# Kernel optimization log

Hardware: AMD Instinct MI355X
Metric: run time of the kernel (lower is better)

The kernel has to match this reference:

```python
import jax, jax.numpy as jnp
import numpy as np

N_NODES = 100000
N_EDGES = 1600000
F_IN_N = 64
F_IN_E = 64
F_OUT_N = 64
F_OUT_E = 64


def setup_inputs() -> dict:
    key = jax.random.key(0)
    ks = jax.random.split(key, 10)
    nfeats = jax.random.normal(ks[0], (N_NODES, F_IN_N), dtype=jnp.float32)
    efeats = jax.random.normal(ks[1], (N_EDGES, F_IN_E), dtype=jnp.float32)
    src = jax.random.randint(ks[2], (N_EDGES,), 0, N_NODES, dtype=jnp.int32)
    dst = jax.random.randint(ks[3], (N_EDGES,), 0, N_NODES, dtype=jnp.int32)
    s = 0.05
    W_node = jax.random.normal(ks[4], (F_OUT_N, F_IN_N), dtype=jnp.float32) * s
    b_node = jnp.zeros((F_OUT_N,), dtype=jnp.float32)
    W_ni = jax.random.normal(ks[5], (F_OUT_E, F_IN_N), dtype=jnp.float32) * s
    W_nj = jax.random.normal(ks[6], (F_OUT_E, F_IN_N), dtype=jnp.float32) * s
    W_fij = jax.random.normal(ks[7], (F_OUT_E, F_IN_E), dtype=jnp.float32) * s
    bias = jnp.zeros((F_OUT_E,), dtype=jnp.float32)
    return {"nfeats": nfeats, "efeats": efeats, "src": src, "dst": dst,
            "W_node": W_node, "b_node": b_node, "W_ni": W_ni, "W_nj": W_nj,
            "W_fij": W_fij, "bias": bias}


def reference(nfeats, efeats, src, dst, W_node, b_node, W_ni, W_nj, W_fij, bias):
    # edge update: leaky_relu(f_ni[src] + f_nj[dst] + f_fij + bias)
    f_ni = nfeats @ W_ni.T        # [N, Fe]
    f_nj = nfeats @ W_nj.T        # [N, Fe]
    f_fij = efeats @ W_fij.T      # [E, Fe]
    f_out = jax.nn.leaky_relu(f_ni[src] + f_nj[dst] + f_fij + bias, negative_slope=0.01)
    # node update: mean over in-edges of transformed source features
    h = nfeats @ W_node.T + b_node                      # [N, Fn]
    msg_sum = jax.ops.segment_sum(h[src], dst, num_segments=N_NODES)   # [N, Fn]
    deg = jax.ops.segment_sum(jnp.ones((src.shape[0],), dtype=h.dtype), dst,
                              num_segments=N_NODES)
    h_out = msg_sum / jnp.maximum(deg, 1.0)[:, None]    # 0 for isolated nodes
    return (h_out, f_out)
```

## Files before the change

kernel.cpp:

```cpp
#include <hip/hip_runtime.h>

#define NN 100000
#define NE 1600000
#define F 64
#define NSB ((NN + 255) / 256)
#define NTB ((NN + 127) / 128)

typedef float f32x4 __attribute__((ext_vector_type(4)));
typedef short bf16x8 __attribute__((ext_vector_type(8)));

__device__ inline unsigned short f2bf(float f) {
    unsigned u = __builtin_bit_cast(unsigned, f);
    u = (u + 0x7fffu + ((u >> 16) & 1u)) >> 16;
    return (unsigned short)u;
}
__device__ inline float bf2f(unsigned short b) { return __builtin_bit_cast(float, (unsigned)b << 16); }
__device__ inline float bflo(unsigned u) { return __builtin_bit_cast(float, u << 16); }
__device__ inline float bfhi(unsigned u) { return __builtin_bit_cast(float, u & 0xffff0000u); }

__device__ inline bf16x8 pack8(const f32x4 v0, const f32x4 v1) {
    bf16x8 pk;
    pk[0] = (short)f2bf(v0[0]); pk[1] = (short)f2bf(v0[1]);
    pk[2] = (short)f2bf(v0[2]); pk[3] = (short)f2bf(v0[3]);
    pk[4] = (short)f2bf(v1[0]); pk[5] = (short)f2bf(v1[1]);
    pk[6] = (short)f2bf(v1[2]); pk[7] = (short)f2bf(v1[3]);
    return pk;
}

__global__ __launch_bounds__(256, 2) void node_kernel(
    const float* __restrict__ nfeats,
    const float* __restrict__ W_node, const float* __restrict__ b_node,
    const float* __restrict__ W_ni,   const float* __restrict__ W_nj,
    unsigned short* __restrict__ f_ni16, unsigned short* __restrict__ f_nj16,
    unsigned short* __restrict__ h16, int* __restrict__ counts)
{
    __shared__ bf16x8 As8[128 * 8];
    __shared__ bf16x8 Ws8[64 * 8];
    float* Df = reinterpret_cast<float*>(As8);

    const int t = threadIdx.x;
    const int w = t >> 6, lane = t & 63;
    const int tile0 = blockIdx.x * 128;
    const int m = blockIdx.y;

    if (m == 0 && t < 128 && tile0 + t < NN) counts[tile0 + t] = 0;

    {
        const float* Wp = (m == 0) ? W_ni : (m == 1) ? W_nj : W_node;
        const f32x4* gw = reinterpret_cast<const f32x4*>(Wp);
#pragma unroll
        for (int i = 0; i < 2; ++i) {
            const int c = i * 256 + t;
            const int row = c >> 3, slot = c & 7;
            Ws8[row * 8 + (slot ^ (row & 7))] = pack8(gw[2 * c], gw[2 * c + 1]);
        }
    }
    {
        const f32x4* gsrc = reinterpret_cast<const f32x4*>(nfeats + (size_t)tile0 * F);
#pragma unroll
        for (int i = 0; i < 4; ++i) {
            const int c = i * 256 + t;
            const int row = c >> 3, slot = c & 7;
            f32x4 v0 = f32x4{0.f, 0.f, 0.f, 0.f}, v1 = f32x4{0.f, 0.f, 0.f, 0.f};
            if (tile0 + row < NN) { v0 = gsrc[2 * c]; v1 = gsrc[2 * c + 1]; }
            As8[row * 8 + (slot ^ (row & 7))] = pack8(v0, v1);
        }
    }
    __syncthreads();

    bf16x8 af[2][2];
#pragma unroll
    for (int mt = 0; mt < 2; ++mt)
#pragma unroll
        for (int ks = 0; ks < 2; ++ks) {
            const int row = w * 32 + mt * 16 + (lane & 15);
            const int kslot = ks * 4 + (lane >> 4);
            af[mt][ks] = As8[row * 8 + (kslot ^ (row & 7))];
        }

    bf16x8 bfr[4][2];
#pragma unroll
    for (int nt = 0; nt < 4; ++nt)
#pragma unroll
        for (int ks = 0; ks < 2; ++ks) {
            const int c = nt * 16 + (lane & 15);
            const int kslot = ks * 4 + (lane >> 4);
            bfr[nt][ks] = Ws8[c * 8 + (kslot ^ (c & 7))];
        }

    f32x4 acc[2][4];
#pragma unroll
    for (int mt = 0; mt < 2; ++mt)
#pragma unroll
        for (int nt = 0; nt < 4; ++nt) acc[mt][nt] = f32x4{0.f, 0.f, 0.f, 0.f};
#pragma unroll
    for (int ks = 0; ks < 2; ++ks)
#pragma unroll
        for (int mt = 0; mt < 2; ++mt)
#pragma unroll
            for (int nt = 0; nt < 4; ++nt)
                acc[mt][nt] = __builtin_amdgcn_mfma_f32_16x16x32_bf16(
                    af[mt][ks], bfr[nt][ks], acc[mt][nt], 0, 0, 0);

    __syncthreads();

    unsigned short* outp = (m == 0) ? f_ni16 : (m == 1) ? f_nj16 : h16;

#pragma unroll
    for (int half = 0; half < 2; ++half) {
#pragma unroll
        for (int mt = 0; mt < 2; ++mt)
#pragma unroll
            for (int ntl = 0; ntl < 2; ++ntl) {
#pragma unroll
                for (int r = 0; r < 4; ++r) {
                    const int row = w * 32 + mt * 16 + (lane >> 4) * 4 + r;
                    const int col = ntl * 16 + (lane & 15);
                    float v = acc[mt][half * 2 + ntl][r];
                    if (m == 2) v += b_node[half * 32 + col];
                    Df[row * 32 + ((col + row) & 31)] = v;
                }
            }
        __syncthreads();

#pragma unroll
        for (int i = 0; i < 2; ++i) {
            const int idx = i * 256 + t;
            const int row = idx >> 2;
            const int c8 = (idx & 3) << 3;
            if (tile0 + row < NN) {
                const float* b = Df + row * 32;
                uint4 pk;
                unsigned u[4];
#pragma unroll
                for (int p = 0; p < 4; ++p) {
                    const unsigned lo = f2bf(b[(c8 + 2 * p + 0 + row) & 31]);
                    const unsigned hi = f2bf(b[(c8 + 2 * p + 1 + row) & 31]);
                    u[p] = lo | (hi << 16);
                }
                pk.x = u[0]; pk.y = u[1]; pk.z = u[2]; pk.w = u[3];
                *reinterpret_cast<uint4*>(outp + (size_t)(tile0 + row) * F + half * 32 + c8) = pk;
            }
        }
        __syncthreads();
    }
}

__global__ __launch_bounds__(256) void edge_kernel(
    const float* __restrict__ efeats,
    const int* __restrict__ src, const int* __restrict__ dst,
    const unsigned short* __restrict__ f_ni16, const unsigned short* __restrict__ f_nj16,
    const float* __restrict__ W_fij, const float* __restrict__ bias,
    float* __restrict__ f_out, int* __restrict__ counts)
{
    __shared__ bf16x8 As8[256 * 8];
    __shared__ bf16x8 Ws8[64 * 8];
    float* Df = reinterpret_cast<float*>(As8);

    const int t = threadIdx.x;
    const int w = t >> 6, lane = t & 63;
    const int tile0 = blockIdx.x * 256;
    const int e = tile0 + t;
    const int s = src[e], d = dst[e];

    atomicAdd(&counts[d], 1);

    {
        const f32x4* gw = reinterpret_cast<const f32x4*>(W_fij);
#pragma unroll
        for (int i = 0; i < 2; ++i) {
            const int c = i * 256 + t;
            const int row = c >> 3, slot = c & 7;
            Ws8[row * 8 + (slot ^ (row & 7))] = pack8(gw[2 * c], gw[2 * c + 1]);
        }
    }
    {
        const f32x4* gsrc = reinterpret_cast<const f32x4*>(efeats + (size_t)tile0 * F);
#pragma unroll
        for (int i = 0; i < 8; ++i) {
            const int c = i * 256 + t;
            const int row = c >> 3, slot = c & 7;
            const f32x4 v0 = __builtin_nontemporal_load(gsrc + 2 * c);
            const f32x4 v1 = __builtin_nontemporal_load(gsrc + 2 * c + 1);
            As8[row * 8 + (slot ^ (row & 7))] = pack8(v0, v1);
        }
    }
    const uint4* gi = reinterpret_cast<const uint4*>(f_ni16 + (size_t)s * F);
    const uint4* gj = reinterpret_cast<const uint4*>(f_nj16 + (size_t)d * F);
    uint4 vni[4], vnj[4];
#pragma unroll
    for (int i = 0; i < 4; ++i) { vni[i] = gi[i]; vnj[i] = gj[i]; }

    __syncthreads();

    bf16x8 af[4][2], bfr[4][2];
#pragma unroll
    for (int mt = 0; mt < 4; ++mt)
#pragma unroll
        for (int ks = 0; ks < 2; ++ks) {
            const int row = w * 64 + mt * 16 + (lane & 15);
            const int kslot = ks * 4 + (lane >> 4);
            af[mt][ks] = As8[row * 8 + (kslot ^ (row & 7))];
        }
#pragma unroll
    for (int nt = 0; nt < 4; ++nt)
#pragma unroll
        for (int ks = 0; ks < 2; ++ks) {
            const int c = nt * 16 + (lane & 15);
            const int kslot = ks * 4 + (lane >> 4);
            bfr[nt][ks] = Ws8[c * 8 + (kslot ^ (c & 7))];
        }

    f32x4 acc[4][4];
#pragma unroll
    for (int mt = 0; mt < 4; ++mt)
#pragma unroll
        for (int nt = 0; nt < 4; ++nt) acc[mt][nt] = f32x4{0.f, 0.f, 0.f, 0.f};

#pragma unroll
    for (int ks = 0; ks < 2; ++ks)
#pragma unroll
        for (int mt = 0; mt < 4; ++mt)
#pragma unroll
            for (int nt = 0; nt < 4; ++nt)
                acc[mt][nt] = __builtin_amdgcn_mfma_f32_16x16x32_bf16(
                    af[mt][ks], bfr[nt][ks], acc[mt][nt], 0, 0, 0);

    __syncthreads();

    f32x4* gout = reinterpret_cast<f32x4*>(f_out + (size_t)tile0 * F);

#pragma unroll
    for (int half = 0; half < 2; ++half) {
#pragma unroll
        for (int mt = 0; mt < 4; ++mt)
#pragma unroll
            for (int ntl = 0; ntl < 2; ++ntl) {
                const int nt = half * 2 + ntl;
#pragma unroll
                for (int r = 0; r < 4; ++r) {
                    const int row = w * 64 + mt * 16 + (lane >> 4) * 4 + r;
                    const int col = ntl * 16 + (lane & 15);
                    Df[row * 32 + ((col + row) & 31)] = acc[mt][nt][r];
                }
            }
        uint4 nni[4], nnj[4];
        if (half == 0) {
#pragma unroll
            for (int i = 0; i < 4; ++i) { nni[i] = gi[4 + i]; nnj[i] = gj[4 + i]; }
        }
        __syncthreads();

        float* rb = Df + t * 32;
#pragma unroll
        for (int c = 0; c < 32; ++c) {
            float v = rb[(c + t) & 31];
            const unsigned wi = vni[c >> 3][(c >> 1) & 3];
            const unsigned wj = vnj[c >> 3][(c >> 1) & 3];
            v += (c & 1) ? bfhi(wi) : bflo(wi);
            v += (c & 1) ? bfhi(wj) : bflo(wj);
            v += bias[half * 32 + c];
            v = (v > 0.f) ? v : 0.01f * v;
            rb[(c + t) & 31] = v;
        }
        __syncthreads();

#pragma unroll
        for (int i = 0; i < 8; ++i) {
            const int idx = i * 256 + t;
            const int row = idx >> 3;
            const int c4 = (idx & 7) << 2;
            const float* b = Df + row * 32;
            f32x4 v;
            v[0] = b[(c4 + 0 + row) & 31];
            v[1] = b[(c4 + 1 + row) & 31];
            v[2] = b[(c4 + 2 + row) & 31];
            v[3] = b[(c4 + 3 + row) & 31];
            __builtin_nontemporal_store(v, gout + row * 16 + half * 8 + (idx & 7));
        }
        if (half == 0) {
            __syncthreads();
#pragma unroll
            for (int i = 0; i < 4; ++i) { vni[i] = nni[i]; vnj[i] = nnj[i]; }
        }
    }
}

__global__ __launch_bounds__(256) void scan1_kernel(
    const int* __restrict__ counts, int* __restrict__ offsets, int* __restrict__ blocksums)
{
    __shared__ int sd[256];
    const int t = threadIdx.x;
    const int i = blockIdx.x * 256 + t;
    const int v = (i < NN) ? counts[i] : 0;
    sd[t] = v;
    __syncthreads();
#pragma unroll
    for (int off = 1; off < 256; off <<= 1) {
        const int x = (t >= off) ? sd[t - off] : 0;
        __syncthreads();
        sd[t] += x;
        __syncthreads();
    }
    if (i < NN) offsets[i] = sd[t] - v;
    if (t == 255) blocksums[blockIdx.x] = sd[255];
}

__global__ __launch_bounds__(512) void scan2_kernel(
    const int* __restrict__ blocksums, int* __restrict__ blockpref)
{
    __shared__ int sd[512];
    const int t = threadIdx.x;
    const int v = (t < NSB) ? blocksums[t] : 0;
    sd[t] = v;
    __syncthreads();
#pragma unroll
    for (int off = 1; off < 512; off <<= 1) {
        const int x = (t >= off) ? sd[t - off] : 0;
        __syncthreads();
        sd[t] += x;
        __syncthreads();
    }
    if (t < NSB) blockpref[t] = sd[t] - v;
}

__global__ __launch_bounds__(256) void scan3_kernel(
    int* __restrict__ offsets, const int* __restrict__ blockpref, int* __restrict__ cursor)
{
    const int i = blockIdx.x * 256 + threadIdx.x;
    if (i < NN) {
        const int o = offsets[i] + blockpref[blockIdx.x];
        offsets[i] = o;
        cursor[i] = o;
    }
    if (i == 0) offsets[NN] = NE;
}

__global__ __launch_bounds__(256) void place_kernel(
    const int* __restrict__ src, const int* __restrict__ dst,
    int* __restrict__ cursor, int* __restrict__ eidx)
{
    const int e = blockIdx.x * 256 + threadIdx.x;
    if (e >= NE) return;
    const int pos = atomicAdd(&cursor[dst[e]], 1);
    eidx[pos] = src[e];
}

__global__ __launch_bounds__(256) void gather_kernel(
    const unsigned short* __restrict__ h16, const int* __restrict__ offsets,
    const int* __restrict__ eidx, float* __restrict__ h_out)
{
    const int n = blockIdx.x * 4 + (threadIdx.x >> 6);
    const int lane = threadIdx.x & 63;
    if (n >= NN) return;
    const int beg = offsets[n], end = offsets[n + 1];
    float acc = 0.f;
    int k = beg;
    for (; k + 4 <= end; k += 4) {
        const int s0 = eidx[k], s1 = eidx[k + 1], s2 = eidx[k + 2], s3 = eidx[k + 3];
        const float v0 = bf2f(h16[(size_t)s0 * F + lane]);
        const float v1 = bf2f(h16[(size_t)s1 * F + lane]);
        const float v2 = bf2f(h16[(size_t)s2 * F + lane]);
        const float v3 = bf2f(h16[(size_t)s3 * F + lane]);
        acc += v0; acc += v1; acc += v2; acc += v3;
    }
    for (; k < end; ++k) acc += bf2f(h16[(size_t)eidx[k] * F + lane]);
    const float deg = (float)(end - beg);
    __builtin_nontemporal_store(acc / fmaxf(deg, 1.0f), h_out + (size_t)n * F + lane);
}

extern "C" void kernel_launch(void* const* d_in, const int* in_sizes, int n_in,
                              void* d_out, int out_size, void* d_ws, size_t ws_size,
                              hipStream_t stream)
{
    const float* nfeats = (const float*)d_in[0];
    const float* efeats = (const float*)d_in[1];
    const int*   src    = (const int*)  d_in[2];
    const int*   dst    = (const int*)  d_in[3];
    const float* W_node = (const float*)d_in[4];
    const float* b_node = (const float*)d_in[5];
    const float* W_ni   = (const float*)d_in[6];
    const float* W_nj   = (const float*)d_in[7];
    const float* W_fij  = (const float*)d_in[8];
    const float* bias   = (const float*)d_in[9];

    float* h_out = (float*)d_out;
    float* f_out = (float*)d_out + (size_t)NN * F;

    unsigned short* f_ni16 = (unsigned short*)d_ws;
    unsigned short* f_nj16 = f_ni16 + (size_t)NN * F;
    unsigned short* h16    = f_nj16 + (size_t)NN * F;
    int*   offsets = (int*)(h16 + (size_t)NN * F);
    int*   cursor  = offsets + (NN + 1);
    int*   counts  = cursor + NN;
    int*   eidx    = counts + NN;
    int*   blocksums = eidx + NE;
    int*   blockpref = blocksums + NSB;
    const size_t need = ((size_t)3 * NN * F) * sizeof(unsigned short)
                      + ((size_t)(3 * NN + 1) + NE + 2 * NSB) * sizeof(int);
    if (ws_size < need) return;

    node_kernel<<<dim3(NTB, 3), 256, 0, stream>>>(nfeats, W_node, b_node, W_ni, W_nj,
                                                  f_ni16, f_nj16, h16, counts);
    edge_kernel<<<NE / 256, 256, 0, stream>>>(efeats, src, dst, f_ni16, f_nj16, W_fij, bias,
                                              f_out, counts);
    scan1_kernel<<<NSB, 256, 0, stream>>>(counts, offsets, blocksums);
    scan2_kernel<<<1, 512, 0, stream>>>(blocksums, blockpref);
    scan3_kernel<<<NSB, 256, 0, stream>>>(offsets, blockpref, cursor);
    place_kernel<<<(NE + 255) / 256, 256, 0, stream>>>(src, dst, cursor, eidx);
    gather_kernel<<<(NN + 3) / 4, 256, 0, stream>>>(h16, offsets, eidx, h_out);
}
```

Before: 432.7 us.

## Split edge GEMM by output half to cut registers; pair-load gather rows

The edge kernel now computes the MFMA product one 32-column half at a time and loads the matching f_ni/f_nj row slices inside each half. This shrinks the live accumulator and fragment registers, and the launch bounds now request 3 blocks per CU to raise occupancy. The cost is losing the prefetch of gather rows ahead of the GEMM, plus an extra barrier per half. Separately, the node gather kernel has each half-wave read 32-bit bf16 pairs for different edges and combines the halves with a cross-lane shuffle, halving the load instructions per row.

```diff
diff --git a/kernel.cpp b/kernel.cpp
--- a/kernel.cpp
+++ b/kernel.cpp
@@ -7,6 +7,7 @@
 #define NTB ((NN + 127) / 128)
 
 typedef float f32x4 __attribute__((ext_vector_type(4)));
+typedef float f32x2 __attribute__((ext_vector_type(2)));
 typedef short bf16x8 __attribute__((ext_vector_type(8)));
 
 __device__ inline unsigned short f2bf(float f) {
@@ -146,7 +147,7 @@
     }
 }
 
-__global__ __launch_bounds__(256) void edge_kernel(
+__global__ __launch_bounds__(256, 3) void edge_kernel(
     const float* __restrict__ efeats,
     const int* __restrict__ src, const int* __restrict__ dst,
     const unsigned short* __restrict__ f_ni16, const unsigned short* __restrict__ f_nj16,
@@ -162,8 +163,6 @@
     const int tile0 = blockIdx.x * 256;
     const int e = tile0 + t;
     const int s = src[e], d = dst[e];
-
-    atomicAdd(&counts[d], 1);
 
     {
         const f32x4* gw = reinterpret_cast<const f32x4*>(W_fij);
@@ -185,15 +184,10 @@
             As8[row * 8 + (slot ^ (row & 7))] = pack8(v0, v1);
         }
     }
-    const uint4* gi = reinterpret_cast<const uint4*>(f_ni16 + (size_t)s * F);
-    const uint4* gj = reinterpret_cast<const uint4*>(f_nj16 + (size_t)d * F);
-    uint4 vni[4], vnj[4];
-#pragma unroll
-    for (int i = 0; i < 4; ++i) { vni[i] = gi[i]; vnj[i] = gj[i]; }
-
+    atomicAdd(&counts[d], 1);
     __syncthreads();
 
-    bf16x8 af[4][2], bfr[4][2];
+    bf16x8 af[4][2];
 #pragma unroll
     for (int mt = 0; mt < 4; ++mt)
 #pragma unroll
@@ -202,53 +196,53 @@
             const int kslot = ks * 4 + (lane >> 4);
             af[mt][ks] = As8[row * 8 + (kslot ^ (row & 7))];
         }
-#pragma unroll
-    for (int nt = 0; nt < 4; ++nt)
-#pragma unroll
-        for (int ks = 0; ks < 2; ++ks) {
-            const int c = nt * 16 + (lane & 15);
-            const int kslot = ks * 4 + (lane >> 4);
-            bfr[nt][ks] = Ws8[c * 8 + (kslot ^ (c & 7))];
-        }
-
-    f32x4 acc[4][4];
-#pragma unroll
-    for (int mt = 0; mt < 4; ++mt)
-#pragma unroll
-        for (int nt = 0; nt < 4; ++nt) acc[mt][nt] = f32x4{0.f, 0.f, 0.f, 0.f};
-
-#pragma unroll
-    for (int ks = 0; ks < 2; ++ks)
+
+    const uint4* gi = reinterpret_cast<const uint4*>(f_ni16 + (size_t)s * F);
+    const uint4* gj = reinterpret_cast<const uint4*>(f_nj16 + (size_t)d * F);
+    f32x4* gout = reinterpret_cast<f32x4*>(f_out + (size_t)tile0 * F);
+
+#pragma unroll
+    for (int half = 0; half < 2; ++half) {
+        bf16x8 bfr[2][2];
+#pragma unroll
+        for (int ntl = 0; ntl < 2; ++ntl)
+#pragma unroll
+            for (int ks = 0; ks < 2; ++ks) {
+                const int c = (half * 2 + ntl) * 16 + (lane & 15);
+                const int kslot = ks * 4 + (lane >> 4);
+                bfr[ntl][ks] = Ws8[c * 8 + (kslot ^ (c & 7))];
+            }
+        uint4 vni[4], vnj[4];
+#pragma unroll
+        for (int i = 0; i < 4; ++i) { vni[i] = gi[half * 4 + i]; vnj[i] = gj[half * 4 + i]; }
+
+        f32x4 acc[4][2];
 #pragma unroll
         for (int mt = 0; mt < 4; ++mt)
 #pragma unroll
-            for (int nt = 0; nt < 4; ++nt)
-                acc[mt][nt] = __builtin_amdgcn_mfma_f32_16x16x32_bf16(
-                    af[mt][ks], bfr[nt][ks], acc[mt][nt], 0, 0, 0);
-
-    __syncthreads();
-
-    f32x4* gout = reinterpret_cast<f32x4*>(f_out + (size_t)tile0 * F);
-
-#pragma unroll
-    for (int half = 0; half < 2; ++half) {
+            for (int ntl = 0; ntl < 2; ++ntl) acc[mt][ntl] = f32x4{0.f, 0.f, 0.f, 0.f};
+#pragma unroll
+        for (int ks = 0; ks < 2; ++ks)
+#pragma unroll
+            for (int mt = 0; mt < 4; ++mt)
+#pragma unroll
+                for (int ntl = 0; ntl < 2; ++ntl)
+                    acc[mt][ntl] = __builtin_amdgcn_mfma_f32_16x16x32_bf16(
+                        af[mt][ks], bfr[ntl][ks], acc[mt][ntl], 0, 0, 0);
+
+        __syncthreads();
+
 #pragma unroll
         for (int mt = 0; mt < 4; ++mt)
 #pragma unroll
             for (int ntl = 0; ntl < 2; ++ntl) {
-                const int nt = half * 2 + ntl;
 #pragma unroll
                 for (int r = 0; r < 4; ++r) {
                     const int row = w * 64 + mt * 16 + (lane >> 4) * 4 + r;
                     const int col = ntl * 16 + (lane & 15);
-                    Df[row * 32 + ((col + row) & 31)] = acc[mt][nt][r];
+                    Df[row * 32 + ((col + row) & 31)] = acc[mt][ntl][r];
                 }
             }
-        uint4 nni[4], nnj[4];
-        if (half == 0) {
-#pragma unroll
-            for (int i = 0; i < 4; ++i) { nni[i] = gi[4 + i]; nnj[i] = gj[4 + i]; }
-        }
         __syncthreads();
 
         float* rb = Df + t * 32;
@@ -278,11 +272,7 @@
             v[3] = b[(c4 + 3 + row) & 31];
             __builtin_nontemporal_store(v, gout + row * 16 + half * 8 + (idx & 7));
         }
-        if (half == 0) {
-            __syncthreads();
-#pragma unroll
-            for (int i = 0; i < 4; ++i) { vni[i] = nni[i]; vnj[i] = nnj[i]; }
-        }
+        __syncthreads();
     }
 }
 
@@ -354,19 +344,39 @@
     const int lane = threadIdx.x & 63;
     if (n >= NN) return;
     const int beg = offsets[n], end = offsets[n + 1];
-    float acc = 0.f;
+    const int colp = (lane & 31) * 2;
+    const int sel = lane >> 5;
+    float a0 = 0.f, a1 = 0.f;
     int k = beg;
     for (; k + 4 <= end; k += 4) {
-        const int s0 = eidx[k], s1 = eidx[k + 1], s2 = eidx[k + 2], s3 = eidx[k + 3];
-        const float v0 = bf2f(h16[(size_t)s0 * F + lane]);
-        const float v1 = bf2f(h16[(size_t)s1 * F + lane]);
-        const float v2 = bf2f(h16[(size_t)s2 * F + lane]);
-        const float v3 = bf2f(h16[(size_t)s3 * F + lane]);
-        acc += v0; acc += v1; acc += v2; acc += v3;
-    }
-    for (; k < end; ++k) acc += bf2f(h16[(size_t)eidx[k] * F + lane]);
-    const float deg = (float)(end - beg);
-    __builtin_nontemporal_store(acc / fmaxf(deg, 1.0f), h_out + (size_t)n * F + lane);
+        const int e0 = eidx[k + sel];
+        const int e1 = eidx[k + 2 + sel];
+        const unsigned u0 = *reinterpret_cast<const unsigned*>(h16 + (size_t)e0 * F + colp);
+        const unsigned u1 = *reinterpret_cast<const unsigned*>(h16 + (size_t)e1 * F + colp);
+        a0 += bflo(u0) + bflo(u1);
+        a1 += bfhi(u0) + bfhi(u1);
+    }
+    for (; k + 2 <= end; k += 2) {
+        const int e0 = eidx[k + sel];
+        const unsigned u0 = *reinterpret_cast<const unsigned*>(h16 + (size_t)e0 * F + colp);
+        a0 += bflo(u0);
+        a1 += bfhi(u0);
+    }
+    if (k < end && sel == 0) {
+        const int e0 = eidx[k];
+        const unsigned u0 = *reinterpret_cast<const unsigned*>(h16 + (size_t)e0 * F + colp);
+        a0 += bflo(u0);
+        a1 += bfhi(u0);
+    }
+    a0 += __shfl_xor(a0, 32, 64);
+    a1 += __shfl_xor(a1, 32, 64);
+    if (sel == 0) {
+        const float dg = fmaxf((float)(end - beg), 1.0f);
+        f32x2 o;
+        o[0] = a0 / dg;
+        o[1] = a1 / dg;
+        __builtin_nontemporal_store(o, reinterpret_cast<f32x2*>(h_out + (size_t)n * F + colp));
+    }
 }
 
 extern "C" void kernel_launch(void* const* d_in, const int* in_sizes, int n_in,
```

Result: slower. 466.3 us (+7.8%).
